# Performance work log

Hardware: AMD Instinct MI355X
Metric: run time of the kernel (lower is better)

Reference implementation:

```python
import jax, jax.numpy as jnp
import numpy as np

ALPHA = 0.4
EPS = 1e-5


def setup_inputs() -> dict:
    key = jax.random.key(0)
    features = jax.random.normal(key, (32, 1024, 512), dtype=jnp.float32)
    return {"features": features}


def reference(features):
    B, dim, M = features.shape
    # x_pow2 = x @ x^T / (2M), shape [B, dim, dim]
    x_pow2 = jnp.einsum('bdm,bem->bde', features, features) / (2.0 * M)
    # I_M.bmm(x_pow2*I) broadcasts the diagonal along rows; (x_pow2*I).bmm(I_M) along cols
    diag = jnp.diagonal(x_pow2, axis1=1, axis2=2)  # [B, dim]
    dcov = diag[:, None, :] + diag[:, :, None] - 2.0 * x_pow2
    dcov = jnp.maximum(dcov, 0.0)
    dcov = jnp.power(dcov + EPS, ALPHA)
    # double-centering: the ones/dim matmuls are exactly row/col/total means
    row_mean = jnp.mean(dcov, axis=2, keepdims=True)   # dcov.bmm(I_M/dim)
    col_mean = jnp.mean(dcov, axis=1, keepdims=True)   # (I_M/dim).bmm(dcov)
    tot_mean = jnp.mean(dcov, axis=(1, 2), keepdims=True)
    out = dcov - row_mean - col_mean + tot_mean        # [B, dim, dim]
    # triuvec: upper-triangular (incl. diagonal) entries, row-major order
    idx = np.nonzero(np.triu(np.ones((dim, dim), dtype=np.float32)).reshape(-1))[0]
    return out.reshape(B, dim * dim)[:, idx]
```

## Files before the change

### kernel.cpp

```cpp
#include <hip/hip_runtime.h>
#include <hip/hip_bf16.h>

#define B_ 32
#define D_ 1024
#define M_ 512
#define OUTROW 524800
#define ALPHA_ 0.4f
#define EPS_ 1e-5f

typedef __bf16 bf16x8 __attribute__((ext_vector_type(8)));
typedef float f32x4 __attribute__((ext_vector_type(4)));

__global__ __launch_bounds__(256) void prep_kernel(
    const float* __restrict__ feat, __bf16* __restrict__ featbf,
    float* __restrict__ diag, float* __restrict__ rowsum,
    float* __restrict__ totals)
{
    if (blockIdx.x < 128) {
        rowsum[blockIdx.x * 256 + threadIdx.x] = 0.0f;
        if (blockIdx.x == 0 && threadIdx.x < B_) totals[threadIdx.x] = 0.0f;
    }

    const int w = threadIdx.x >> 6, l = threadIdx.x & 63;
    const int row = blockIdx.x * 4 + w;
    const float4* fp = (const float4*)(feat + (size_t)row * M_);
    float4 v0 = fp[l * 2];
    float4 v1 = fp[l * 2 + 1];
    bf16x8 h;
    h[0] = (__bf16)v0.x; h[1] = (__bf16)v0.y; h[2] = (__bf16)v0.z; h[3] = (__bf16)v0.w;
    h[4] = (__bf16)v1.x; h[5] = (__bf16)v1.y; h[6] = (__bf16)v1.z; h[7] = (__bf16)v1.w;
    *(bf16x8*)(featbf + (size_t)row * M_ + l * 8) = h;
    float s = v0.x*v0.x + v0.y*v0.y + v0.z*v0.z + v0.w*v0.w
            + v1.x*v1.x + v1.y*v1.y + v1.z*v1.z + v1.w*v1.w;
    #pragma unroll
    for (int off = 32; off; off >>= 1) s += __shfl_down(s, off);
    if (l == 0) diag[row] = s * (1.0f / (2.0f * M_));
}

__global__ __launch_bounds__(256, 3) void gram_kernel(
    const __bf16* __restrict__ feat, const float* __restrict__ diag,
    float* __restrict__ out, float* __restrict__ rowsum,
    float* __restrict__ totals)
{
    __shared__ __bf16 As[3][512 * 8];
    __shared__ __bf16 Bs[3][512 * 8];

    const int t = threadIdx.x;
    const int w = t >> 6, l = t & 63;
    const int quad = l >> 4, l15 = l & 15;

    const int L = blockIdx.x;
    const int xcd = L & 7;
    const int slot = L >> 3;
    const int b = xcd + 8 * (slot / 36);
    int u = slot % 36, ti = 0;
    while (u >= 8 - ti) { u -= 8 - ti; ti++; }
    const int tj = ti + u;
    const bool diagTile = (ti == tj);

    const __bf16* Ab = feat + (size_t)b * (D_ * M_) + (size_t)ti * 128 * M_;
    const __bf16* Bb = feat + (size_t)b * (D_ * M_) + (size_t)tj * 128 * M_;

    const int wm = w >> 1, wn = w & 1;

    const int gi0 = ti * 128 + wm * 64;
    const int gj0 = tj * 128 + wn * 64;
    const float* diagB = diag + b * D_;
    float di[4][4], dj[4];
    #pragma unroll
    for (int mi = 0; mi < 4; ++mi)
        #pragma unroll
        for (int r = 0; r < 4; ++r)
            di[mi][r] = diagB[gi0 + mi * 16 + quad * 4 + r];
    #pragma unroll
    for (int nj = 0; nj < 4; ++nj)
        dj[nj] = diagB[gj0 + nj * 16 + l15];

    f32x4 acc[4][4] = {};

    auto stage = [&](int s, int sb) {
        const int koff = s * 32;
        #pragma unroll
        for (int it = 0; it < 2; ++it) {
            const int idx = it * 256 + t;
            const int row = idx >> 2;
            const int cg = (idx & 3) ^ ((row >> 1) & 3);
            const __bf16* ga = Ab + row * M_ + koff + cg * 8;
            const __bf16* gb = Bb + row * M_ + koff + cg * 8;
            __builtin_amdgcn_global_load_lds(
                (const __attribute__((address_space(1))) void*)ga,
                (__attribute__((address_space(3))) void*)(&As[sb][(it * 256 + w * 64) * 8]),
                16, 0, 0);
            __builtin_amdgcn_global_load_lds(
                (const __attribute__((address_space(1))) void*)gb,
                (__attribute__((address_space(3))) void*)(&Bs[sb][(it * 256 + w * 64) * 8]),
                16, 0, 0);
        }
    };

    stage(0, 0);
    stage(1, 1);
    int rb = 0, sn = 2;
    for (int k0 = 0; k0 < 16; ++k0) {
        if (k0 < 15) asm volatile("s_waitcnt vmcnt(4)" ::: "memory");
        else         asm volatile("s_waitcnt vmcnt(0)" ::: "memory");
        __builtin_amdgcn_s_barrier();
        __builtin_amdgcn_sched_barrier(0);
        if (k0 + 2 < 16) stage(k0 + 2, sn);

        bf16x8 af[4], bfr[4];
        #pragma unroll
        for (int mi = 0; mi < 4; ++mi) {
            const int row = wm * 64 + mi * 16 + l15;
            af[mi] = *(const bf16x8*)(&As[rb][(row * 4 + (quad ^ ((row >> 1) & 3))) * 8]);
        }
        #pragma unroll
        for (int nj = 0; nj < 4; ++nj) {
            const int row = wn * 64 + nj * 16 + l15;
            bfr[nj] = *(const bf16x8*)(&Bs[rb][(row * 4 + (quad ^ ((row >> 1) & 3))) * 8]);
        }
        __builtin_amdgcn_s_setprio(1);
        #pragma unroll
        for (int mi = 0; mi < 4; ++mi)
            #pragma unroll
            for (int nj = 0; nj < 4; ++nj)
                acc[mi][nj] = __builtin_amdgcn_mfma_f32_16x16x32_bf16(
                    af[mi], bfr[nj], acc[mi][nj], 0, 0, 0);
        __builtin_amdgcn_s_setprio(0);
        rb = (rb == 2) ? 0 : rb + 1;
        sn = (sn == 2) ? 0 : sn + 1;
    }

    float* outB = out + (size_t)b * OUTROW;
    float rs[4][4] = {};
    float cs[4] = {};
    float wt = 0.f;
    const float invK = 1.0f / 512.0f;

    #pragma unroll
    for (int mi = 0; mi < 4; ++mi) {
        #pragma unroll
        for (int nj = 0; nj < 4; ++nj) {
            const f32x4 a = acc[mi][nj];
            const int j = gj0 + nj * 16 + l15;
            #pragma unroll
            for (int r = 0; r < 4; ++r) {
                const int i = gi0 + mi * 16 + quad * 4 + r;
                float d = di[mi][r] + dj[nj] - a[r] * invK;
                if (i == j) d = 0.0f;
                d = fmaxf(d, 0.0f);
                const float p = __builtin_exp2f(ALPHA_ * __builtin_log2f(d + EPS_));
                rs[mi][r] += p;
                cs[nj] += p;
                wt += p;
                if (!diagTile || j >= i)
                    __builtin_nontemporal_store(
                        p, &outB[(size_t)i * D_ - ((size_t)i * (i + 1)) / 2 + j]);
            }
        }
    }

    #pragma unroll
    for (int mi = 0; mi < 4; ++mi) {
        #pragma unroll
        for (int r = 0; r < 4; ++r) {
            float v = rs[mi][r];
            v += __shfl_xor(v, 1); v += __shfl_xor(v, 2);
            v += __shfl_xor(v, 4); v += __shfl_xor(v, 8);
            if (l15 == 0)
                unsafeAtomicAdd(&rowsum[b * D_ + gi0 + mi * 16 + quad * 4 + r], v);
        }
    }
    if (!diagTile) {
        #pragma unroll
        for (int nj = 0; nj < 4; ++nj) {
            float v = cs[nj];
            v += __shfl_xor(v, 16); v += __shfl_xor(v, 32);
            if (quad == 0)
                unsafeAtomicAdd(&rowsum[b * D_ + gj0 + nj * 16 + l15], v);
        }
    }
    float v = wt;
    #pragma unroll
    for (int off = 32; off; off >>= 1) v += __shfl_down(v, off);
    if (l == 0) unsafeAtomicAdd(&totals[b], diagTile ? v : 2.0f * v);
}

__global__ __launch_bounds__(256) void center_kernel(
    float* __restrict__ out, const float* __restrict__ rowsum,
    const float* __restrict__ totals)
{
    const int b = blockIdx.y;
    const float* rsB = rowsum + b * D_;
    const float tm = totals[b] * (1.0f / ((float)D_ * (float)D_));
    #pragma unroll
    for (int h = 0; h < 2; ++h) {
        const int i = h ? (D_ - 1 - (int)blockIdx.x) : (int)blockIdx.x;
        const float rmi = rsB[i] * (1.0f / D_);
        float* row = out + (size_t)b * OUTROW + (size_t)i * D_ - ((size_t)i * (i + 1)) / 2;
        for (int j = i + (int)threadIdx.x; j < D_; j += 256) {
            float v = __builtin_nontemporal_load(&row[j]);
            __builtin_nontemporal_store(v - rmi - rsB[j] * (1.0f / D_) + tm, &row[j]);
        }
    }
}

extern "C" void kernel_launch(void* const* d_in, const int* in_sizes, int n_in,
                              void* d_out, int out_size, void* d_ws, size_t ws_size,
                              hipStream_t stream) {
    const float* feat = (const float*)d_in[0];
    float* out = (float*)d_out;

    char* ws = (char*)d_ws;
    __bf16* featbf = (__bf16*)ws;
    float* diag    = (float*)(ws + 33554432);
    float* rowsum  = (float*)(ws + 33554432 + 131072);
    float* totals  = (float*)(ws + 33554432 + 262144);

    prep_kernel<<<dim3((B_ * D_) / 4), dim3(256), 0, stream>>>(feat, featbf, diag,
                                                               rowsum, totals);
    gram_kernel<<<dim3(36 * B_), dim3(256), 0, stream>>>(featbf, diag, out, rowsum, totals);
    center_kernel<<<dim3(D_ / 2, B_), dim3(256), 0, stream>>>(out, rowsum, totals);
}
```

Before: 227.7 us.

## Replace LDS-staged block GEMM with per-wave 64x64 tiles loading directly from global

The Gram kernel stops staging 128x128 block tiles through a triple-buffered LDS pipeline with barriers. Each wave now owns an independent 64x64 upper-triangular tile and loads its bf16 fragments straight from global memory into registers, double-buffered in registers. This removes the LDS traffic and block-wide synchronization and changes the grid decomposition. In exchange it gives up operand reuse across waves and relies on L2 for uncoalesced 16-byte row-strided loads. Nontemporal load and store hints are also dropped in favour of plain accesses.

Measured after the change: 266.4 us. 17.0% more time.

```diff
diff --git a/kernel.cpp b/kernel.cpp
--- a/kernel.cpp
+++ b/kernel.cpp
@@ -37,14 +37,27 @@
     if (l == 0) diag[row] = s * (1.0f / (2.0f * M_));
 }
 
-__global__ __launch_bounds__(256, 3) void gram_kernel(
+#define LOADFR(AB, BB, K)                                                    \
+    { _Pragma("unroll")                                                      \
+      for (int f = 0; f < 4; ++f) {                                          \
+          AB[f] = *(const bf16x8*)(pa + (size_t)f * (16 * M_) + (K) * 32);   \
+          BB[f] = *(const bf16x8*)(pb + (size_t)f * (16 * M_) + (K) * 32);   \
+      } }
+
+#define MFMAS(AB, BB)                                                        \
+    { _Pragma("unroll")                                                      \
+      for (int mi = 0; mi < 4; ++mi) {                                       \
+          _Pragma("unroll")                                                  \
+          for (int nj = 0; nj < 4; ++nj)                                     \
+              acc[mi][nj] = __builtin_amdgcn_mfma_f32_16x16x32_bf16(         \
+                  AB[mi], BB[nj], acc[mi][nj], 0, 0, 0);                     \
+      } }
+
+__global__ __launch_bounds__(256) void gram_kernel(
     const __bf16* __restrict__ feat, const float* __restrict__ diag,
     float* __restrict__ out, float* __restrict__ rowsum,
     float* __restrict__ totals)
 {
-    __shared__ __bf16 As[3][512 * 8];
-    __shared__ __bf16 Bs[3][512 * 8];
-
     const int t = threadIdx.x;
     const int w = t >> 6, l = t & 63;
     const int quad = l >> 4, l15 = l & 15;
@@ -52,19 +65,33 @@
     const int L = blockIdx.x;
     const int xcd = L & 7;
     const int slot = L >> 3;
-    const int b = xcd + 8 * (slot / 36);
-    int u = slot % 36, ti = 0;
-    while (u >= 8 - ti) { u -= 8 - ti; ti++; }
+    const int b = xcd + 8 * (slot / 34);
+    const int tile = (slot % 34) * 4 + w;
+    int u = tile, ti = 0;
+    while (u >= 16 - ti) { u -= 16 - ti; ti++; }
     const int tj = ti + u;
     const bool diagTile = (ti == tj);
 
-    const __bf16* Ab = feat + (size_t)b * (D_ * M_) + (size_t)ti * 128 * M_;
-    const __bf16* Bb = feat + (size_t)b * (D_ * M_) + (size_t)tj * 128 * M_;
+    const __bf16* Ab = feat + (size_t)b * (D_ * M_) + (size_t)ti * 64 * M_;
+    const __bf16* Bb = feat + (size_t)b * (D_ * M_) + (size_t)tj * 64 * M_;
 
-    const int wm = w >> 1, wn = w & 1;
+    const __bf16* pa = Ab + (size_t)l15 * M_ + quad * 8;
+    const __bf16* pb = Bb + (size_t)l15 * M_ + quad * 8;
 
-    const int gi0 = ti * 128 + wm * 64;
-    const int gj0 = tj * 128 + wn * 64;
+    f32x4 acc[4][4] = {};
+    bf16x8 a0[4], b0[4], a1[4], b1[4];
+
+    LOADFR(a0, b0, 0);
+    #pragma unroll
+    for (int kk = 0; kk < 8; ++kk) {
+        LOADFR(a1, b1, 2 * kk + 1);
+        MFMAS(a0, b0);
+        if (kk < 7) LOADFR(a0, b0, 2 * kk + 2);
+        MFMAS(a1, b1);
+    }
+
+    const int gi0 = ti * 64;
+    const int gj0 = tj * 64;
     const float* diagB = diag + b * D_;
     float di[4][4], dj[4];
     #pragma unroll
@@ -75,61 +102,6 @@
     #pragma unroll
     for (int nj = 0; nj < 4; ++nj)
         dj[nj] = diagB[gj0 + nj * 16 + l15];
-
-    f32x4 acc[4][4] = {};
-
-    auto stage = [&](int s, int sb) {
-        const int koff = s * 32;
-        #pragma unroll
-        for (int it = 0; it < 2; ++it) {
-            const int idx = it * 256 + t;
-            const int row = idx >> 2;
-            const int cg = (idx & 3) ^ ((row >> 1) & 3);
-            const __bf16* ga = Ab + row * M_ + koff + cg * 8;
-            const __bf16* gb = Bb + row * M_ + koff + cg * 8;
-            __builtin_amdgcn_global_load_lds(
-                (const __attribute__((address_space(1))) void*)ga,
-                (__attribute__((address_space(3))) void*)(&As[sb][(it * 256 + w * 64) * 8]),
-                16, 0, 0);
-            __builtin_amdgcn_global_load_lds(
-                (const __attribute__((address_space(1))) void*)gb,
-                (__attribute__((address_space(3))) void*)(&Bs[sb][(it * 256 + w * 64) * 8]),
-                16, 0, 0);
-        }
-    };
-
-    stage(0, 0);
-    stage(1, 1);
-    int rb = 0, sn = 2;
-    for (int k0 = 0; k0 < 16; ++k0) {
-        if (k0 < 15) asm volatile("s_waitcnt vmcnt(4)" ::: "memory");
-        else         asm volatile("s_waitcnt vmcnt(0)" ::: "memory");
-        __builtin_amdgcn_s_barrier();
-        __builtin_amdgcn_sched_barrier(0);
-        if (k0 + 2 < 16) stage(k0 + 2, sn);
-
-        bf16x8 af[4], bfr[4];
-        #pragma unroll
-        for (int mi = 0; mi < 4; ++mi) {
-            const int row = wm * 64 + mi * 16 + l15;
-            af[mi] = *(const bf16x8*)(&As[rb][(row * 4 + (quad ^ ((row >> 1) & 3))) * 8]);
-        }
-        #pragma unroll
-        for (int nj = 0; nj < 4; ++nj) {
-            const int row = wn * 64 + nj * 16 + l15;
-            bfr[nj] = *(const bf16x8*)(&Bs[rb][(row * 4 + (quad ^ ((row >> 1) & 3))) * 8]);
-        }
-        __builtin_amdgcn_s_setprio(1);
-        #pragma unroll
-        for (int mi = 0; mi < 4; ++mi)
-            #pragma unroll
-            for (int nj = 0; nj < 4; ++nj)
-                acc[mi][nj] = __builtin_amdgcn_mfma_f32_16x16x32_bf16(
-                    af[mi], bfr[nj], acc[mi][nj], 0, 0, 0);
-        __builtin_amdgcn_s_setprio(0);
-        rb = (rb == 2) ? 0 : rb + 1;
-        sn = (sn == 2) ? 0 : sn + 1;
-    }
 
     float* outB = out + (size_t)b * OUTROW;
     float rs[4][4] = {};
@@ -154,8 +126,7 @@
                 cs[nj] += p;
                 wt += p;
                 if (!diagTile || j >= i)
-                    __builtin_nontemporal_store(
-                        p, &outB[(size_t)i * D_ - ((size_t)i * (i + 1)) / 2 + j]);
+                    outB[(size_t)i * D_ - ((size_t)i * (i + 1)) / 2 + j] = p;
             }
         }
     }
@@ -199,8 +170,7 @@
         const float rmi = rsB[i] * (1.0f / D_);
         float* row = out + (size_t)b * OUTROW + (size_t)i * D_ - ((size_t)i * (i + 1)) / 2;
         for (int j = i + (int)threadIdx.x; j < D_; j += 256) {
-            float v = __builtin_nontemporal_load(&row[j]);
-            __builtin_nontemporal_store(v - rmi - rsB[j] * (1.0f / D_) + tm, &row[j]);
+            row[j] = row[j] - rmi - rsB[j] * (1.0f / D_) + tm;
         }
     }
 }
@@ -219,6 +189,6 @@
 
     prep_kernel<<<dim3((B_ * D_) / 4), dim3(256), 0, stream>>>(feat, featbf, diag,
                                                                rowsum, totals);
-    gram_kernel<<<dim3(36 * B_), dim3(256), 0, stream>>>(featbf, diag, out, rowsum, totals);
+    gram_kernel<<<dim3(8 * 136), dim3(256), 0, stream>>>(featbf, diag, out, rowsum, totals);
     center_kernel<<<dim3(D_ / 2, B_), dim3(256), 0, stream>>>(out, rowsum, totals);
 }
```
